# Optimization experiments

Measured on AMD Instinct MI355X. Metric: run time of the kernel, lower is better.

Reference implementation:

```python
import jax, jax.numpy as jnp
import numpy as np

B, S, D, V, ND = 8, 512, 1024, 32000, 8


def setup_inputs() -> dict:
    key = jax.random.key(0)
    k1, k2, k3, k4 = jax.random.split(key, 4)
    scale = 0.02
    return {
        "hidden_states": jax.random.normal(k1, (B, S, D), dtype=jnp.float32),
        "domain_ids": jax.random.randint(k2, (B,), 0, ND + 1),  # index ND triggers default head
        "W_base": jax.random.normal(k3, (D, D), dtype=jnp.float32) * scale,
        "b_base": jnp.zeros((D,), dtype=jnp.float32),
        # slots 0..ND-1 are domain heads, slot ND is the default head
        "W_heads": jax.random.normal(k4, (ND + 1, D, V), dtype=jnp.float32) * scale,
        "b_heads": jnp.zeros((ND + 1, V), dtype=jnp.float32),
    }


def reference(hidden_states, domain_ids, W_base, b_base, W_heads, b_heads):
    # base_projection: Linear(D, D)
    hidden = jnp.einsum("bsd,de->bse", hidden_states, W_base) + b_base
    num_domains = W_heads.shape[0] - 1
    # out-of-range domain ids fall back to the default head (last slot)
    idx = jnp.where((domain_ids >= 0) & (domain_ids < num_domains), domain_ids, num_domains)
    Wg = W_heads[idx]              # [B, D, V] gathered per-example head weights
    bg = b_heads[idx]              # [B, V]
    out = jnp.einsum("bsd,bdv->bsv", hidden, Wg) + bg[:, None, :]
    return out
```

## Files before the change

kernel.cpp:

```cpp
#include <hip/hip_runtime.h>
#include <hip/hip_bf16.h>


#define BCNT 8
#define SLEN 512
#define DDIM 1024
#define VDIM 32000
#define NDOM 8

typedef __attribute__((ext_vector_type(4))) float f32x4;
typedef __attribute__((ext_vector_type(8))) short bf16x8;

static __device__ __forceinline__ unsigned short f2bf(float f) {
    union { float f; unsigned int u; } x; x.f = f;
    unsigned int u = x.u;
    return (unsigned short)((u + 0x7FFFu + ((u >> 16) & 1u)) >> 16);
}

static __device__ __forceinline__ unsigned int pack2(float lo, float hi) {
    float2 t; t.x = lo; t.y = hi;
    union { __hip_bfloat162 h; unsigned int u; } c;
    c.h = __float22bfloat162_rn(t);
    return c.u;
}

#define SBAR()   __builtin_amdgcn_s_barrier()
#define SCHED0() __builtin_amdgcn_sched_barrier(0)

__global__ __launch_bounds__(256)
void gemm1_k(const float* __restrict__ Af, const float* __restrict__ Bbase,
             const float* __restrict__ bias, __hip_bfloat16* __restrict__ Cb,
             int Mrows)
{
    __shared__ __align__(16) __hip_bfloat16 lds_a[128 * 64];
    __shared__ __align__(16) unsigned int   lds_b[32 * 128];

    const int tid  = threadIdx.x;
    const int lane = tid & 63;
    const int w    = tid >> 6;

    const int nwg = gridDim.x;
    const int bid = blockIdx.x;
    const int q   = nwg >> 3;
    const int sid = (bid & 7) * q + (bid >> 3);

    const int MT = Mrows >> 7;
    const int mt = sid % MT;
    const int nt = sid / MT;
    const int m0 = mt << 7;
    const int n0 = nt << 7;

    f32x4 acc[4][4];
    #pragma unroll
    for (int m = 0; m < 4; ++m)
        #pragma unroll
        for (int n = 0; n < 4; ++n)
            acc[m][n] = (f32x4)0.0f;

    const int wr = w >> 1, wc = w & 1;
    const int lr = lane & 15, lg = lane >> 4;

    for (int kt = 0; kt < DDIM / 64; ++kt) {
        const int kbase = kt * 64;

        #pragma unroll
        for (int t = 0; t < 8; ++t) {
            const int flat = (t * 256 + tid) * 4;
            const int row = flat >> 6, col = flat & 63;
            const float4 v = *(const float4*)(Af + (size_t)(m0 + row) * DDIM + kbase + col);
            uint2 pp;
            pp.x = pack2(v.x, v.y);
            pp.y = pack2(v.z, v.w);
            *(uint2*)(lds_a + flat) = pp;
        }

        #pragma unroll
        for (int t = 0; t < 4; ++t) {
            const int id = t * 256 + tid;
            const int kk = id >> 5;
            const int n  = (id & 31) << 2;
            const float* b0 = Bbase + (size_t)(kbase + 2 * kk) * DDIM + n0 + n;
            const float4 e = *(const float4*)b0;
            const float4 o = *(const float4*)(b0 + DDIM);
            uint4 pw;
            pw.x = pack2(e.x, o.x);
            pw.y = pack2(e.y, o.y);
            pw.z = pack2(e.z, o.z);
            pw.w = pack2(e.w, o.w);
            const int ns = n ^ ((kk & 4) << 2);
            *(uint4*)&lds_b[kk * 128 + ns] = pw;
        }

        __syncthreads();

        #pragma unroll
        for (int ks = 0; ks < 2; ++ks) {
            bf16x8 af[4], bfr[4];
            #pragma unroll
            for (int m = 0; m < 4; ++m) {
                const int row = wr * 64 + m * 16 + lr;
                const int k   = ks * 32 + lg * 8;
                af[m] = *(const bf16x8*)&lds_a[row * 64 + k];
            }
            #pragma unroll
            for (int n = 0; n < 4; ++n) {
                const int col = wc * 64 + n * 16 + lr;
                const int kkb = ks * 16 + lg * 4;
                union { unsigned int u[4]; bf16x8 v; } cvt;
                #pragma unroll
                for (int j = 0; j < 4; ++j) {
                    const int kk = kkb + j;
                    const int ns = col ^ ((kk & 4) << 2);
                    cvt.u[j] = lds_b[kk * 128 + ns];
                }
                bfr[n] = cvt.v;
            }
            #pragma unroll
            for (int m = 0; m < 4; ++m)
                #pragma unroll
                for (int n = 0; n < 4; ++n)
                    acc[m][n] = __builtin_amdgcn_mfma_f32_16x16x32_bf16(af[m], bfr[n], acc[m][n], 0, 0, 0);
        }

        __syncthreads();
    }

    #pragma unroll
    for (int m = 0; m < 4; ++m) {
        #pragma unroll
        for (int n = 0; n < 4; ++n) {
            const int col = n0 + wc * 64 + n * 16 + lr;
            const float bv = bias[col];
            #pragma unroll
            for (int r = 0; r < 4; ++r) {
                const int row = m0 + wr * 64 + m * 16 + lg * 4 + r;
                Cb[(size_t)row * DDIM + col] = __hip_bfloat16_raw{f2bf(acc[m][n][r] + bv)};
            }
        }
    }
}

__global__ __launch_bounds__(512, 4)
void gemm2_k(const __hip_bfloat16* __restrict__ A, const float* __restrict__ Wh,
             const float* __restrict__ bh, float* __restrict__ out,
             const int* __restrict__ dom)
{
    __shared__ __align__(16) __hip_bfloat16 ldsA[256 * 64];
    __shared__ __align__(16) unsigned int   ldsB[128 * 32];

    const int tid  = threadIdx.x;
    const int lane = tid & 63;
    const int w    = tid >> 6;
    const int wr   = w >> 1;
    const int wc   = w & 1;
    const int lr   = lane & 15;
    const int lg   = lane >> 4;

    const int bid = blockIdx.x;
    const int ex  = bid / 500;
    const int r   = bid % 500;
    const int mt  = r & 1;
    const int nt  = r >> 1;
    const int m0  = ex * SLEN + mt * 256;
    const int n0  = nt * 128;

    const int di  = dom[ex];
    const int hid = (di >= 0 && di < NDOM) ? di : NDOM;
    const float* Bp   = Wh + (size_t)hid * DDIM * (size_t)VDIM;
    const float* bias = bh + (size_t)hid * (size_t)VDIM;

    f32x4 acc[4][4];
    #pragma unroll
    for (int m = 0; m < 4; ++m)
        #pragma unroll
        for (int n = 0; n < 4; ++n)
            acc[m][n] = (f32x4)0.0f;

    const int nb  = (tid & 63) << 1;
    const int kb  = (tid >> 6) << 3;
    const int qb  = kb >> 1;
    const int bsw = (lane & 7) << 2;
    const int bslot = qb ^ bsw;

    float2 br[8];

    #define LOADB(KT) do {                                                         \
        const float* _p = Bp + (size_t)((KT) * 64 + kb) * VDIM + n0 + nb;          \
        _Pragma("unroll")                                                          \
        for (int j = 0; j < 8; ++j) br[j] = *(const float2*)(_p + (size_t)j * VDIM); \
    } while (0)

    #define WRITEB() do {                                                          \
        uint4 w0, w1;                                                              \
        w0.x = pack2(br[0].x, br[1].x); w0.y = pack2(br[2].x, br[3].x);            \
        w0.z = pack2(br[4].x, br[5].x); w0.w = pack2(br[6].x, br[7].x);            \
        w1.x = pack2(br[0].y, br[1].y); w1.y = pack2(br[2].y, br[3].y);            \
        w1.z = pack2(br[4].y, br[5].y); w1.w = pack2(br[6].y, br[7].y);            \
        *(uint4*)&ldsB[nb * 32 + bslot]       = w0;                                \
        *(uint4*)&ldsB[(nb + 1) * 32 + bslot] = w1;                                \
    } while (0)

    #define STAGEA(KT) do {                                                        \
        _Pragma("unroll")                                                          \
        for (int i = 0; i < 4; ++i) {                                              \
            const int base_e = (i * 8 + w) * 512;                                  \
            const int flat   = base_e + lane * 8;                                  \
            const int row    = flat >> 6;                                          \
            const int kbyte  = (flat & 63) * 2;                                    \
            const int srck   = (kbyte ^ ((row & 7) << 4)) >> 1;                    \
            const __hip_bfloat16* src = A + (size_t)(m0 + row) * DDIM + (KT) * 64 + srck; \
            __builtin_amdgcn_global_load_lds(                                      \
                (const __attribute__((address_space(1))) unsigned int*)src,        \
                (__attribute__((address_space(3))) unsigned int*)(ldsA + base_e),  \
                16, 0, 0);                                                         \
        }                                                                          \
    } while (0)

    #define COMPUTE() do {                                                         \
        _Pragma("unroll")                                                          \
        for (int ks = 0; ks < 2; ++ks) {                                           \
            bf16x8 af[4], bfr[4];                                                  \
            _Pragma("unroll")                                                      \
            for (int m = 0; m < 4; ++m) {                                          \
                const int row = wr * 64 + m * 16 + lr;                             \
                const int kby = ks * 64 + lg * 16;                                 \
                const int eff = kby ^ ((row & 7) << 4);                            \
                af[m] = *(const bf16x8*)&ldsA[row * 64 + (eff >> 1)];              \
            }                                                                      \
            _Pragma("unroll")                                                      \
            for (int n = 0; n < 4; ++n) {                                          \
                const int col  = wc * 64 + n * 16 + lr;                            \
                const int kkb  = ks * 16 + lg * 4;                                 \
                const int slot = kkb ^ (((col >> 1) & 7) << 2);                    \
                bfr[n] = *(const bf16x8*)&ldsB[col * 32 + slot];                   \
            }                                                                      \
            _Pragma("unroll")                                                      \
            for (int m = 0; m < 4; ++m)                                            \
                _Pragma("unroll")                                                  \
                for (int n = 0; n < 4; ++n)                                        \
                    acc[m][n] = __builtin_amdgcn_mfma_f32_16x16x32_bf16(af[m], bfr[n], acc[m][n], 0, 0, 0); \
        }                                                                          \
    } while (0)

    LOADB(0);
    SCHED0();
    STAGEA(0);
    SCHED0();
    WRITEB();
    SCHED0();
    LOADB(1);
    SCHED0();
    asm volatile("s_waitcnt vmcnt(8) lgkmcnt(0)" ::: "memory");
    SCHED0();
    SBAR();

    for (int kt = 0; kt < 16; ++kt) {
        COMPUTE();
        if (kt < 15) {
            SCHED0();
            SBAR();
            SCHED0();
            STAGEA(kt + 1);
            SCHED0();
            WRITEB();
            SCHED0();
            if (kt < 14) {
                LOADB(kt + 2);
                SCHED0();
                asm volatile("s_waitcnt vmcnt(8) lgkmcnt(0)" ::: "memory");
            } else {
                asm volatile("s_waitcnt vmcnt(0) lgkmcnt(0)" ::: "memory");
            }
            SCHED0();
            SBAR();
        }
    }

    #pragma unroll
    for (int n = 0; n < 4; ++n) {
        const int col = n0 + wc * 64 + n * 16 + lr;
        const float bv = bias[col];
        #pragma unroll
        for (int m = 0; m < 4; ++m) {
            #pragma unroll
            for (int r = 0; r < 4; ++r) {
                const int row = m0 + wr * 64 + m * 16 + lg * 4 + r;
                out[(size_t)row * VDIM + col] = acc[m][n][r] + bv;
            }
        }
    }

    #undef LOADB
    #undef WRITEB
    #undef STAGEA
    #undef COMPUTE
}

extern "C" void kernel_launch(void* const* d_in, const int* in_sizes, int n_in,
                              void* d_out, int out_size, void* d_ws, size_t ws_size,
                              hipStream_t stream)
{
    const float* hs  = (const float*)d_in[0];
    const int*   dom = (const int*)d_in[1];
    const float* Wb  = (const float*)d_in[2];
    const float* bb  = (const float*)d_in[3];
    const float* Wh  = (const float*)d_in[4];
    const float* bh  = (const float*)d_in[5];
    float* out = (float*)d_out;
    __hip_bfloat16* hidden = (__hip_bfloat16*)d_ws;

    const int M = BCNT * SLEN;

    const int g1 = (M / 128) * (DDIM / 128);
    hipLaunchKernelGGL(gemm1_k, dim3(g1), dim3(256), 0, stream, hs, Wb, bb, hidden, M);

    const int g2 = BCNT * (SLEN / 256) * (VDIM / 128);
    hipLaunchKernelGGL(gemm2_k, dim3(g2), dim3(512), 0, stream, hidden, Wh, bh, out, dom);
}
```

Before: 547.8 us.

## Split per-tile MFMA into halves and overlap next-tile staging with second half

The k-tile compute is split into two k-slices. Second-slice fragments are read into registers before the barrier, so the next tile's A staging and B LDS writes can be issued while the second half of the MFMAs runs, with s_setprio raising priority around the MFMA bursts. The B LDS slot swizzle also gains a column-group rotation to reduce bank conflicts, and the read side is updated to match. The cost is more live fragment registers, which could lower occupancy, plus a more fragile ordering of waits and barriers.

Result: slower. 955.2 us (+74.4%).

```diff
diff --git a/kernel.cpp b/kernel.cpp
--- a/kernel.cpp
+++ b/kernel.cpp
@@ -180,7 +180,7 @@
     const int kb  = (tid >> 6) << 3;
     const int qb  = kb >> 1;
     const int bsw = (lane & 7) << 2;
-    const int bslot = qb ^ bsw;
+    const int bslot = ((qb ^ bsw) + (((nb >> 4) & 3) << 3)) & 31;
 
     float2 br[8];
 
@@ -216,30 +216,30 @@
         }                                                                          \
     } while (0)
 
-    #define COMPUTE() do {                                                         \
-        _Pragma("unroll")                                                          \
-        for (int ks = 0; ks < 2; ++ks) {                                           \
-            bf16x8 af[4], bfr[4];                                                  \
+    #define READ_FRAGS(AF, BF, KS) do {                                           \
+        _Pragma("unroll")                                                          \
+        for (int m = 0; m < 4; ++m) {                                              \
+            const int row = wr * 64 + m * 16 + lr;                                 \
+            const int kby = (KS) * 64 + lg * 16;                                   \
+            const int eff = kby ^ ((row & 7) << 4);                                \
+            AF[m] = *(const bf16x8*)&ldsA[row * 64 + (eff >> 1)];                  \
+        }                                                                          \
+        _Pragma("unroll")                                                          \
+        for (int n = 0; n < 4; ++n) {                                              \
+            const int col  = wc * 64 + n * 16 + lr;                                \
+            const int kkb  = (KS) * 16 + lg * 4;                                   \
+            const int slot = ((kkb ^ (((col >> 1) & 7) << 2))                      \
+                              + (((col >> 4) & 3) << 3)) & 31;                     \
+            BF[n] = *(const bf16x8*)&ldsB[col * 32 + slot];                        \
+        }                                                                          \
+    } while (0)
+
+    #define MFMA16(AF, BF) do {                                                    \
+        _Pragma("unroll")                                                          \
+        for (int m = 0; m < 4; ++m)                                                \
             _Pragma("unroll")                                                      \
-            for (int m = 0; m < 4; ++m) {                                          \
-                const int row = wr * 64 + m * 16 + lr;                             \
-                const int kby = ks * 64 + lg * 16;                                 \
-                const int eff = kby ^ ((row & 7) << 4);                            \
-                af[m] = *(const bf16x8*)&ldsA[row * 64 + (eff >> 1)];              \
-            }                                                                      \
-            _Pragma("unroll")                                                      \
-            for (int n = 0; n < 4; ++n) {                                          \
-                const int col  = wc * 64 + n * 16 + lr;                            \
-                const int kkb  = ks * 16 + lg * 4;                                 \
-                const int slot = kkb ^ (((col >> 1) & 7) << 2);                    \
-                bfr[n] = *(const bf16x8*)&ldsB[col * 32 + slot];                   \
-            }                                                                      \
-            _Pragma("unroll")                                                      \
-            for (int m = 0; m < 4; ++m)                                            \
-                _Pragma("unroll")                                                  \
-                for (int n = 0; n < 4; ++n)                                        \
-                    acc[m][n] = __builtin_amdgcn_mfma_f32_16x16x32_bf16(af[m], bfr[n], acc[m][n], 0, 0, 0); \
-        }                                                                          \
+            for (int n = 0; n < 4; ++n)                                            \
+                acc[m][n] = __builtin_amdgcn_mfma_f32_16x16x32_bf16(AF[m], BF[n], acc[m][n], 0, 0, 0); \
     } while (0)
 
     LOADB(0);
@@ -255,22 +255,37 @@
     SBAR();
 
     for (int kt = 0; kt < 16; ++kt) {
-        COMPUTE();
+        bf16x8 af0[4], bf0[4], af1[4], bf1[4];
+
+        READ_FRAGS(af0, bf0, 0);
+        SCHED0();
+        __builtin_amdgcn_s_setprio(1);
+        MFMA16(af0, bf0);
+        __builtin_amdgcn_s_setprio(0);
+        SCHED0();
+
+        READ_FRAGS(af1, bf1, 1);
+        SCHED0();
+        asm volatile("s_waitcnt lgkmcnt(0)" ::: "memory");
+        SCHED0();
         if (kt < 15) {
-            SCHED0();
             SBAR();
             SCHED0();
             STAGEA(kt + 1);
             SCHED0();
             WRITEB();
             SCHED0();
-            if (kt < 14) {
-                LOADB(kt + 2);
-                SCHED0();
-                asm volatile("s_waitcnt vmcnt(8) lgkmcnt(0)" ::: "memory");
-            } else {
-                asm volatile("s_waitcnt vmcnt(0) lgkmcnt(0)" ::: "memory");
-            }
+            if (kt < 14) { LOADB(kt + 2); SCHED0(); }
+        }
+
+        __builtin_amdgcn_s_setprio(1);
+        MFMA16(af1, bf1);
+        __builtin_amdgcn_s_setprio(0);
+        SCHED0();
+
+        if (kt < 15) {
+            if (kt < 14) asm volatile("s_waitcnt vmcnt(8) lgkmcnt(0)" ::: "memory");
+            else         asm volatile("s_waitcnt vmcnt(0) lgkmcnt(0)" ::: "memory");
             SCHED0();
             SBAR();
         }
@@ -283,9 +298,9 @@
         #pragma unroll
         for (int m = 0; m < 4; ++m) {
             #pragma unroll
-            for (int r = 0; r < 4; ++r) {
-                const int row = m0 + wr * 64 + m * 16 + lg * 4 + r;
-                out[(size_t)row * VDIM + col] = acc[m][n][r] + bv;
+            for (int r2 = 0; r2 < 4; ++r2) {
+                const int row = m0 + wr * 64 + m * 16 + lg * 4 + r2;
+                out[(size_t)row * VDIM + col] = acc[m][n][r2] + bv;
             }
         }
     }
@@ -293,7 +308,8 @@
     #undef LOADB
     #undef WRITEB
     #undef STAGEA
-    #undef COMPUTE
+    #undef READ_FRAGS
+    #undef MFMA16
 }
 
 extern "C" void kernel_launch(void* const* d_in, const int* in_sizes, int n_in,
```
